# Optimization experiments

Hardware: AMD Instinct MI355X
Metric: run time of the kernel (lower is better)

## Reference

```python
import jax, jax.numpy as jnp
import numpy as np

B, D, H = 32768, 512, 512


def setup_inputs() -> dict:
    key = jax.random.key(0)
    ks = jax.random.split(key, 20)
    stdv = 1.0 / np.sqrt(H)

    def u(k, shape):
        return jax.random.uniform(k, shape, jnp.float32, -stdv, stdv)

    inp = {
        "input": jax.random.normal(ks[0], (B, D), jnp.float32),
        "h": jax.random.normal(ks[1], (B, H), jnp.float32),
        "c": jax.random.normal(ks[2], (B, H), jnp.float32),
    }
    names = ["w_ii", "w_hi", "b_ii", "b_hi", "w_if", "w_hf", "b_if", "b_hf",
             "w_ig", "w_hg", "b_ig", "b_hg", "w_io", "w_ho", "b_io", "b_ho"]
    shapes = {"w_i": (D, H), "w_h": (H, H), "b_": (H,)}
    for i, n in enumerate(names):
        shp = (D, H) if n.startswith("w_i") else ((H, H) if n.startswith("w_h") else (H,))
        inp[n] = u(ks[3 + i], shp)
    return inp


def lstm_cell(input, h, c,
              w_ii, w_hi, b_ii, b_hi, w_if, w_hf, b_if, b_hf,
              w_ig, w_hg, b_ig, b_hg, w_io, w_ho, b_io, b_ho):
    # Fuse the 8 small GEMMs into 2 concatenated GEMMs: [B,D]@[D,4H], [B,H]@[H,4H].
    w_x = jnp.concatenate([w_ii, w_if, w_ig, w_io], axis=1)   # [D, 4H]
    w_h = jnp.concatenate([w_hi, w_hf, w_hg, w_ho], axis=1)   # [H, 4H]
    b = jnp.concatenate([b_ii + b_hi, b_if + b_hf, b_ig + b_hg, b_io + b_ho])  # [4H]
    pre = input @ w_x + h @ w_h + b                            # [B, 4H]
    i, f, g, o = jnp.split(pre, 4, axis=1)
    i = jax.nn.sigmoid(i)
    f = jax.nn.sigmoid(f)
    g = jax.nn.sigmoid(g)  # NOTE: source code uses sigmoid here (docstring says tanh)
    o = jax.nn.sigmoid(o)
    c_prime = f * c + i * g
    h_prime = o * jnp.tanh(c_prime)
    return h_prime, c_prime


def reference(input, h, c,
              w_ii, w_hi, b_ii, b_hi, w_if, w_hf, b_if, b_hf,
              w_ig, w_hg, b_ig, b_hg, w_io, w_ho, b_io, b_ho):
    return lstm_cell(input, h, c,
                     w_ii, w_hi, b_ii, b_hi, w_if, w_hf, b_if, b_hf,
                     w_ig, w_hg, b_ig, b_hg, w_io, w_ho, b_io, b_ho)
```

## Files before the change

kernel.cpp:

```cpp
#include <hip/hip_runtime.h>
#include <hip/hip_bf16.h>

typedef __attribute__((ext_vector_type(8))) __bf16 bf16x8;
typedef __attribute__((ext_vector_type(4))) float f32x4;

#define NB 32768
#define HDIM 512
#define KDIM 1024

struct WPtrs { const float* wi[4]; const float* wh[4]; };
struct BPtrs { const float* bi[4]; const float* bh[4]; };

__device__ __forceinline__ float fsigmoid(float x) {
  return 1.0f / (1.0f + __expf(-x));
}
__device__ __forceinline__ float ftanh(float x) {
  return 2.0f / (1.0f + __expf(-2.0f * x)) - 1.0f;
}
__device__ __forceinline__ bf16x8 pack8(float4 a, float4 b) {
  bf16x8 r;
  r[0] = (__bf16)a.x; r[1] = (__bf16)a.y; r[2] = (__bf16)a.z; r[3] = (__bf16)a.w;
  r[4] = (__bf16)b.x; r[5] = (__bf16)b.y; r[6] = (__bf16)b.z; r[7] = (__bf16)b.w;
  return r;
}
__device__ __forceinline__ void gll16(const void* g, void* l) {
  __builtin_amdgcn_global_load_lds(
      (const __attribute__((address_space(1))) void*)g,
      (__attribute__((address_space(3))) void*)l, 16, 0, 0);
}
#define MFMA16(A, B, C) \
  C = __builtin_amdgcn_mfma_f32_16x16x32_bf16(A, B, C, 0, 0, 0)
#define SBAR() __builtin_amdgcn_s_barrier()
#define SCHED0() __builtin_amdgcn_sched_barrier(0)

__global__ void pack_bias_kernel(BPtrs p, float* __restrict__ bias) {
  int idx = blockIdx.x * 256 + threadIdx.x;
  int g = idx >> 9, np = idx & 511;
  bias[idx] = p.bi[g][np] + p.bh[g][np];
}

__global__ void conv_a_kernel(const float* __restrict__ x,
                              const float* __restrict__ h,
                              __bf16* __restrict__ Abf) {
  const size_t N8 = (size_t)NB * KDIM / 8;
  for (size_t i = (size_t)blockIdx.x * blockDim.x + threadIdx.x; i < N8;
       i += (size_t)gridDim.x * blockDim.x) {
    size_t e = i * 8;
    int k = (int)(e & (KDIM - 1));
    size_t r = e >> 10;
    const float* s = (k < 512) ? (x + r * 512 + k) : (h + r * 512 + (k - 512));
    float4 v0 = *(const float4*)s;
    float4 v1 = *(const float4*)(s + 4);
    *(bf16x8*)(Abf + e) = pack8(v0, v1);
  }
}

__global__ void pack_w2_kernel(WPtrs p, __bf16* __restrict__ Wt) {
  __shared__ float tile[64][65];
  const int kt = blockIdx.x;
  const int nt = blockIdx.y;
  const int g = blockIdx.z;
  const int k0 = kt * 64, n0 = nt * 64;
  const float* src = (k0 < 512) ? p.wi[g] : p.wh[g];
  const int k0l = (k0 < 512) ? k0 : (k0 - 512);
  const int rr = threadIdx.x >> 6;
  const int cc = threadIdx.x & 63;
#pragma unroll
  for (int pp = 0; pp < 16; ++pp) {
    int kk = pp * 4 + rr;
    tile[kk][cc] = src[(size_t)(k0l + kk) * 512 + (n0 + cc)];
  }
  __syncthreads();
#pragma unroll
  for (int pp = 0; pp < 16; ++pp) {
    int nn = pp * 4 + rr;
    int np = n0 + nn;
    int prow = (np >> 6) * 256 + ((g >> 1) << 7) + (((np >> 4) & 3) << 5) +
               ((g & 1) << 4) + (np & 15);
    Wt[(size_t)prow * KDIM + (k0 + cc)] = (__bf16)tile[cc][nn];
  }
}

__global__ __launch_bounds__(512, 1) void lstm_gemm6(
    const __bf16* __restrict__ Abf, const __bf16* __restrict__ Wt,
    const float* __restrict__ cin, const float* __restrict__ bias,
    float* __restrict__ out) {
  __shared__ alignas(16) char lds[131072];
  const int tid = threadIdx.x;
  const int wid = tid >> 6;
  const int wm = wid >> 2, wn = wid & 3;
  const int lane = tid & 63;
  const int fc = lane & 15, fg = lane >> 4;

  const int bn = blockIdx.x & 7;
  const int bmg = blockIdx.x >> 3;

  const __bf16* Bsrc = Wt + (size_t)(bn * 256) * KDIM;

  const int srow = (wid << 4) + (lane >> 2);
  const int skoff = (lane & 3) * 8;

  f32x4 acc[8][4];
#pragma unroll
  for (int m = 0; m < 8; ++m)
#pragma unroll
    for (int n = 0; n < 4; ++n) acc[m][n] = (f32x4){0.f, 0.f, 0.f, 0.f};

  bf16x8 a[2], b[4];

  auto stA = [&](int t) {
    if (t < 128) {
      const __bf16* s = Abf +
                        ((size_t)((bmg << 2) + (t >> 5)) * 256 + srow) * KDIM +
                        (t & 31) * 32 + skoff;
      uint32_t lb = (uint32_t)(t & 3) * 32768 + (uint32_t)wid * 1024;
      gll16(s, (void*)&lds[lb]);
      gll16(s + (size_t)128 * KDIM, (void*)&lds[lb + 8192]);
    }
  };
  auto stB = [&](int t) {
    if (t < 128) {
      const __bf16* s = Bsrc + (size_t)srow * KDIM + (t & 31) * 32 + skoff;
      uint32_t lb = (uint32_t)(t & 3) * 32768 + 16384 + (uint32_t)wid * 1024;
      gll16(s, (void*)&lds[lb]);
      gll16(s + (size_t)128 * KDIM, (void*)&lds[lb + 8192]);
    }
  };
  auto ldA = [&](uint32_t t3, int mq) -> bf16x8 {
    return *(const bf16x8*)&lds[t3 +
                                (uint32_t)(wm * 128 + mq * 16 + fc) * 64 +
                                (uint32_t)fg * 16];
  };
  auto ldB = [&](uint32_t t3, int nq) -> bf16x8 {
    return *(const bf16x8*)&lds[t3 + 16384 +
                                (uint32_t)((nq >> 1) * 128 + wn * 32 +
                                           (nq & 1) * 16 + fc) * 64 +
                                (uint32_t)fg * 16];
  };

  const int np = bn * 64 + wn * 16 + fc;
  const float bi = bias[np];
  const float bf_ = bias[512 + np];
  const float bg = bias[1024 + np];
  const float bo = bias[1536 + np];
  const size_t couts = (size_t)NB * HDIM;

  stA(0); stB(0); stA(1); stB(1);
  asm volatile("s_waitcnt vmcnt(4)" ::: "memory");
  SBAR();

#pragma unroll 4
  for (int t = 0; t < 128; ++t) {
    const uint32_t t3 = (uint32_t)(t & 3) * 32768;
    a[0] = ldA(t3, 0);
    b[0] = ldB(t3, 0);
    b[1] = ldB(t3, 1);
    b[2] = ldB(t3, 2);
    b[3] = ldB(t3, 3);
    a[1] = ldA(t3, 1);
#pragma unroll
    for (int mq = 0; mq < 8; ++mq) {
      if (mq < 7) {
        asm volatile("s_waitcnt lgkmcnt(1)" ::: "memory");
      } else {
        asm volatile("s_waitcnt lgkmcnt(0)" ::: "memory");
      }
      SCHED0();
      __builtin_amdgcn_s_setprio(1);
      MFMA16(a[mq & 1], b[0], acc[mq][0]);
      MFMA16(a[mq & 1], b[1], acc[mq][1]);
      MFMA16(a[mq & 1], b[2], acc[mq][2]);
      MFMA16(a[mq & 1], b[3], acc[mq][3]);
      __builtin_amdgcn_s_setprio(0);
      if (mq < 6) a[mq & 1] = ldA(t3, mq + 2);
      if (mq == 2) stA(t + 2);
      if (mq == 4) stB(t + 2);
    }
    if (t < 126) {
      asm volatile("s_waitcnt vmcnt(4)" ::: "memory");
    } else if (t == 126) {
      asm volatile("s_waitcnt vmcnt(0)" ::: "memory");
    }
    SBAR();

    if ((t & 31) == 31) {
      const int grp = t >> 5;
#pragma unroll
      for (int mf = 0; mf < 8; ++mf) {
        const int grow0 = ((bmg << 2) + grp) * 256 + wm * 128 + mf * 16 + fg * 4;
#pragma unroll
        for (int j = 0; j < 4; ++j) {
          const size_t off = (size_t)(grow0 + j) * HDIM + np;
          float i_ = fsigmoid(acc[mf][0][j] + bi);
          float f_ = fsigmoid(acc[mf][1][j] + bf_);
          float g_ = fsigmoid(acc[mf][2][j] + bg);
          float o_ = fsigmoid(acc[mf][3][j] + bo);
          float cp = f_ * cin[off] + i_ * g_;
          out[off] = o_ * ftanh(cp);
          out[couts + off] = cp;
        }
#pragma unroll
        for (int n = 0; n < 4; ++n) acc[mf][n] = (f32x4){0.f, 0.f, 0.f, 0.f};
      }
    }
  }
}

extern "C" void kernel_launch(void* const* d_in, const int* in_sizes, int n_in,
                              void* d_out, int out_size, void* d_ws,
                              size_t ws_size, hipStream_t stream) {
  const float* xin = (const float*)d_in[0];
  const float* hin = (const float*)d_in[1];
  const float* cin = (const float*)d_in[2];
  WPtrs wp;
  wp.wi[0] = (const float*)d_in[3];
  wp.wi[1] = (const float*)d_in[7];
  wp.wi[2] = (const float*)d_in[11];
  wp.wi[3] = (const float*)d_in[15];
  wp.wh[0] = (const float*)d_in[4];
  wp.wh[1] = (const float*)d_in[8];
  wp.wh[2] = (const float*)d_in[12];
  wp.wh[3] = (const float*)d_in[16];
  BPtrs bp;
  bp.bi[0] = (const float*)d_in[5];
  bp.bi[1] = (const float*)d_in[9];
  bp.bi[2] = (const float*)d_in[13];
  bp.bi[3] = (const float*)d_in[17];
  bp.bh[0] = (const float*)d_in[6];
  bp.bh[1] = (const float*)d_in[10];
  bp.bh[2] = (const float*)d_in[14];
  bp.bh[3] = (const float*)d_in[18];

  const size_t needA = (size_t)NB * KDIM * 2;
  const size_t needW = (size_t)2048 * KDIM * 2;

  __bf16* Abf = (__bf16*)d_ws;
  __bf16* Wt = (__bf16*)((char*)d_ws + needA);
  float* bias = (float*)((char*)d_ws + needA + needW);

  conv_a_kernel<<<2048, 256, 0, stream>>>(xin, hin, Abf);
  pack_w2_kernel<<<dim3(16, 8, 4), 256, 0, stream>>>(wp, Wt);
  pack_bias_kernel<<<8, 256, 0, stream>>>(bp, bias);
  lstm_gemm6<<<256, 512, 0, stream>>>(Abf, Wt, cin, bias, (float*)d_out);
}
```

Baseline: 213.8 us.

## Retile LSTM GEMM to 128x128 blocks with swizzled LDS and two blocks per CU

Measured after the change: 232.7 us. 1.09x slower.

```diff
diff --git a/kernel.cpp b/kernel.cpp
--- a/kernel.cpp
+++ b/kernel.cpp
@@ -32,6 +32,7 @@
   C = __builtin_amdgcn_mfma_f32_16x16x32_bf16(A, B, C, 0, 0, 0)
 #define SBAR() __builtin_amdgcn_s_barrier()
 #define SCHED0() __builtin_amdgcn_sched_barrier(0)
+#define LGKM(n) asm volatile("s_waitcnt lgkmcnt(" #n ")" ::: "memory")
 
 __global__ void pack_bias_kernel(BPtrs p, float* __restrict__ bias) {
   int idx = blockIdx.x * 256 + threadIdx.x;
@@ -55,7 +56,7 @@
   }
 }
 
-__global__ void pack_w2_kernel(WPtrs p, __bf16* __restrict__ Wt) {
+__global__ void pack_w3_kernel(WPtrs p, __bf16* __restrict__ Wt) {
   __shared__ float tile[64][65];
   const int kt = blockIdx.x;
   const int nt = blockIdx.y;
@@ -75,119 +76,147 @@
   for (int pp = 0; pp < 16; ++pp) {
     int nn = pp * 4 + rr;
     int np = n0 + nn;
-    int prow = (np >> 6) * 256 + ((g >> 1) << 7) + (((np >> 4) & 3) << 5) +
-               ((g & 1) << 4) + (np & 15);
+    int prow = ((np >> 4) << 6) + (g << 4) + (np & 15);
     Wt[(size_t)prow * KDIM + (k0 + cc)] = (__bf16)tile[cc][nn];
   }
 }
 
-__global__ __launch_bounds__(512, 1) void lstm_gemm6(
+__global__ __launch_bounds__(256, 2) void lstm_gemm7(
     const __bf16* __restrict__ Abf, const __bf16* __restrict__ Wt,
     const float* __restrict__ cin, const float* __restrict__ bias,
     float* __restrict__ out) {
-  __shared__ alignas(16) char lds[131072];
+  __shared__ alignas(16) char lds[65536];
   const int tid = threadIdx.x;
   const int wid = tid >> 6;
-  const int wm = wid >> 2, wn = wid & 3;
+  const int wm = wid >> 1, wn = wid & 1;
   const int lane = tid & 63;
   const int fc = lane & 15, fg = lane >> 4;
 
-  const int bn = blockIdx.x & 7;
-  const int bmg = blockIdx.x >> 3;
-
-  const __bf16* Bsrc = Wt + (size_t)(bn * 256) * KDIM;
-
-  const int srow = (wid << 4) + (lane >> 2);
-  const int skoff = (lane & 3) * 8;
-
-  f32x4 acc[8][4];
-#pragma unroll
-  for (int m = 0; m < 8; ++m)
+  const int bn = blockIdx.x & 15;
+  const int bmg = blockIdx.x >> 4;
+
+  const __bf16* Bsrc = Wt + (size_t)(bn * 128) * KDIM;
+
+  const int r0 = tid >> 3;
+  const int ssl = ((tid & 7) ^ (r0 & 7)) * 8;
+  const uint32_t ldst0 = (uint32_t)wid * 1024;
+
+  f32x4 acc[4][4];
+#pragma unroll
+  for (int m = 0; m < 4; ++m)
 #pragma unroll
     for (int n = 0; n < 4; ++n) acc[m][n] = (f32x4){0.f, 0.f, 0.f, 0.f};
 
-  bf16x8 a[2], b[4];
+  bf16x8 a0[4], b0[4], a1[4], b1[4];
 
   auto stA = [&](int t) {
     if (t < 128) {
-      const __bf16* s = Abf +
-                        ((size_t)((bmg << 2) + (t >> 5)) * 256 + srow) * KDIM +
-                        (t & 31) * 32 + skoff;
-      uint32_t lb = (uint32_t)(t & 3) * 32768 + (uint32_t)wid * 1024;
+      const int rt = (bmg << 3) + (t >> 4);
+      const __bf16* s =
+          Abf + (size_t)(rt * 128 + r0) * KDIM + (t & 15) * 64 + ssl;
+      uint32_t lb = (uint32_t)(t & 1) * 32768 + ldst0;
       gll16(s, (void*)&lds[lb]);
-      gll16(s + (size_t)128 * KDIM, (void*)&lds[lb + 8192]);
+      gll16(s + (size_t)32 * KDIM, (void*)&lds[lb + 4096]);
+      gll16(s + (size_t)64 * KDIM, (void*)&lds[lb + 8192]);
+      gll16(s + (size_t)96 * KDIM, (void*)&lds[lb + 12288]);
     }
   };
   auto stB = [&](int t) {
     if (t < 128) {
-      const __bf16* s = Bsrc + (size_t)srow * KDIM + (t & 31) * 32 + skoff;
-      uint32_t lb = (uint32_t)(t & 3) * 32768 + 16384 + (uint32_t)wid * 1024;
+      const __bf16* s = Bsrc + (size_t)r0 * KDIM + (t & 15) * 64 + ssl;
+      uint32_t lb = (uint32_t)(t & 1) * 32768 + 16384 + ldst0;
       gll16(s, (void*)&lds[lb]);
-      gll16(s + (size_t)128 * KDIM, (void*)&lds[lb + 8192]);
+      gll16(s + (size_t)32 * KDIM, (void*)&lds[lb + 4096]);
+      gll16(s + (size_t)64 * KDIM, (void*)&lds[lb + 8192]);
+      gll16(s + (size_t)96 * KDIM, (void*)&lds[lb + 12288]);
     }
   };
-  auto ldA = [&](uint32_t t3, int mq) -> bf16x8 {
-    return *(const bf16x8*)&lds[t3 +
-                                (uint32_t)(wm * 128 + mq * 16 + fc) * 64 +
-                                (uint32_t)fg * 16];
-  };
-  auto ldB = [&](uint32_t t3, int nq) -> bf16x8 {
-    return *(const bf16x8*)&lds[t3 + 16384 +
-                                (uint32_t)((nq >> 1) * 128 + wn * 32 +
-                                           (nq & 1) * 16 + fc) * 64 +
-                                (uint32_t)fg * 16];
-  };
-
-  const int np = bn * 64 + wn * 16 + fc;
+  auto ldA = [&](int cb, int mq, int ks) -> bf16x8 {
+    int row = wm * 64 + mq * 16 + fc;
+    uint32_t off = (uint32_t)cb * 32768 + (uint32_t)row * 128 +
+                   (uint32_t)(((ks * 4 + fg) ^ (row & 7)) << 4);
+    return *(const bf16x8*)&lds[off];
+  };
+  auto ldB = [&](int cb, int nq, int ks) -> bf16x8 {
+    int row = wn * 64 + nq * 16 + fc;
+    uint32_t off = (uint32_t)cb * 32768 + 16384 + (uint32_t)row * 128 +
+                   (uint32_t)(((ks * 4 + fg) ^ (row & 7)) << 4);
+    return *(const bf16x8*)&lds[off];
+  };
+
+  const int np = bn * 32 + wn * 16 + fc;
   const float bi = bias[np];
   const float bf_ = bias[512 + np];
   const float bg = bias[1024 + np];
   const float bo = bias[1536 + np];
   const size_t couts = (size_t)NB * HDIM;
 
-  stA(0); stB(0); stA(1); stB(1);
-  asm volatile("s_waitcnt vmcnt(4)" ::: "memory");
+  stA(0);
+  stB(0);
+  asm volatile("s_waitcnt vmcnt(0)" ::: "memory");
   SBAR();
 
-#pragma unroll 4
+#pragma unroll 2
   for (int t = 0; t < 128; ++t) {
-    const uint32_t t3 = (uint32_t)(t & 3) * 32768;
-    a[0] = ldA(t3, 0);
-    b[0] = ldB(t3, 0);
-    b[1] = ldB(t3, 1);
-    b[2] = ldB(t3, 2);
-    b[3] = ldB(t3, 3);
-    a[1] = ldA(t3, 1);
-#pragma unroll
-    for (int mq = 0; mq < 8; ++mq) {
-      if (mq < 7) {
-        asm volatile("s_waitcnt lgkmcnt(1)" ::: "memory");
-      } else {
-        asm volatile("s_waitcnt lgkmcnt(0)" ::: "memory");
-      }
-      SCHED0();
-      __builtin_amdgcn_s_setprio(1);
-      MFMA16(a[mq & 1], b[0], acc[mq][0]);
-      MFMA16(a[mq & 1], b[1], acc[mq][1]);
-      MFMA16(a[mq & 1], b[2], acc[mq][2]);
-      MFMA16(a[mq & 1], b[3], acc[mq][3]);
-      __builtin_amdgcn_s_setprio(0);
-      if (mq < 6) a[mq & 1] = ldA(t3, mq + 2);
-      if (mq == 2) stA(t + 2);
-      if (mq == 4) stB(t + 2);
-    }
-    if (t < 126) {
-      asm volatile("s_waitcnt vmcnt(4)" ::: "memory");
-    } else if (t == 126) {
-      asm volatile("s_waitcnt vmcnt(0)" ::: "memory");
-    }
+    const int cb = t & 1;
+    b0[0] = ldB(cb, 0, 0); b0[1] = ldB(cb, 1, 0);
+    b0[2] = ldB(cb, 2, 0); b0[3] = ldB(cb, 3, 0);
+    a0[0] = ldA(cb, 0, 0); a0[1] = ldA(cb, 1, 0);
+    a0[2] = ldA(cb, 2, 0); a0[3] = ldA(cb, 3, 0);
+    b1[0] = ldB(cb, 0, 1); b1[1] = ldB(cb, 1, 1);
+    b1[2] = ldB(cb, 2, 1); b1[3] = ldB(cb, 3, 1);
+    a1[0] = ldA(cb, 0, 1); a1[1] = ldA(cb, 1, 1);
+    a1[2] = ldA(cb, 2, 1); a1[3] = ldA(cb, 3, 1);
+    LGKM(11); SCHED0();
+    __builtin_amdgcn_s_setprio(1);
+    MFMA16(a0[0], b0[0], acc[0][0]); MFMA16(a0[0], b0[1], acc[0][1]);
+    MFMA16(a0[0], b0[2], acc[0][2]); MFMA16(a0[0], b0[3], acc[0][3]);
+    __builtin_amdgcn_s_setprio(0);
+    LGKM(10); SCHED0();
+    __builtin_amdgcn_s_setprio(1);
+    MFMA16(a0[1], b0[0], acc[1][0]); MFMA16(a0[1], b0[1], acc[1][1]);
+    MFMA16(a0[1], b0[2], acc[1][2]); MFMA16(a0[1], b0[3], acc[1][3]);
+    __builtin_amdgcn_s_setprio(0);
+    stA(t + 1);
+    LGKM(9); SCHED0();
+    __builtin_amdgcn_s_setprio(1);
+    MFMA16(a0[2], b0[0], acc[2][0]); MFMA16(a0[2], b0[1], acc[2][1]);
+    MFMA16(a0[2], b0[2], acc[2][2]); MFMA16(a0[2], b0[3], acc[2][3]);
+    __builtin_amdgcn_s_setprio(0);
+    LGKM(8); SCHED0();
+    __builtin_amdgcn_s_setprio(1);
+    MFMA16(a0[3], b0[0], acc[3][0]); MFMA16(a0[3], b0[1], acc[3][1]);
+    MFMA16(a0[3], b0[2], acc[3][2]); MFMA16(a0[3], b0[3], acc[3][3]);
+    __builtin_amdgcn_s_setprio(0);
+    stB(t + 1);
+    LGKM(3); SCHED0();
+    __builtin_amdgcn_s_setprio(1);
+    MFMA16(a1[0], b1[0], acc[0][0]); MFMA16(a1[0], b1[1], acc[0][1]);
+    MFMA16(a1[0], b1[2], acc[0][2]); MFMA16(a1[0], b1[3], acc[0][3]);
+    __builtin_amdgcn_s_setprio(0);
+    LGKM(2); SCHED0();
+    __builtin_amdgcn_s_setprio(1);
+    MFMA16(a1[1], b1[0], acc[1][0]); MFMA16(a1[1], b1[1], acc[1][1]);
+    MFMA16(a1[1], b1[2], acc[1][2]); MFMA16(a1[1], b1[3], acc[1][3]);
+    __builtin_amdgcn_s_setprio(0);
+    LGKM(1); SCHED0();
+    __builtin_amdgcn_s_setprio(1);
+    MFMA16(a1[2], b1[0], acc[2][0]); MFMA16(a1[2], b1[1], acc[2][1]);
+    MFMA16(a1[2], b1[2], acc[2][2]); MFMA16(a1[2], b1[3], acc[2][3]);
+    __builtin_amdgcn_s_setprio(0);
+    LGKM(0); SCHED0();
+    __builtin_amdgcn_s_setprio(1);
+    MFMA16(a1[3], b1[0], acc[3][0]); MFMA16(a1[3], b1[1], acc[3][1]);
+    MFMA16(a1[3], b1[2], acc[3][2]); MFMA16(a1[3], b1[3], acc[3][3]);
+    __builtin_amdgcn_s_setprio(0);
+    asm volatile("s_waitcnt vmcnt(0)" ::: "memory");
     SBAR();
 
-    if ((t & 31) == 31) {
-      const int grp = t >> 5;
-#pragma unroll
-      for (int mf = 0; mf < 8; ++mf) {
-        const int grow0 = ((bmg << 2) + grp) * 256 + wm * 128 + mf * 16 + fg * 4;
+    if ((t & 15) == 15) {
+      const int rt = (bmg << 3) + (t >> 4);
+#pragma unroll
+      for (int mf = 0; mf < 4; ++mf) {
+        const int grow0 = rt * 128 + wm * 64 + mf * 16 + fg * 4;
 #pragma unroll
         for (int j = 0; j < 4; ++j) {
           const size_t off = (size_t)(grow0 + j) * HDIM + np;
@@ -239,7 +268,7 @@
   float* bias = (float*)((char*)d_ws + needA + needW);
 
   conv_a_kernel<<<2048, 256, 0, stream>>>(xin, hin, Abf);
-  pack_w2_kernel<<<dim3(16, 8, 4), 256, 0, stream>>>(wp, Wt);
+  pack_w3_kernel<<<dim3(16, 8, 4), 256, 0, stream>>>(wp, Wt);
   pack_bias_kernel<<<8, 256, 0, stream>>>(bp, bias);
-  lstm_gemm6<<<256, 512, 0, stream>>>(Abf, Wt, cin, bias, (float*)d_out);
-}
+  lstm_gemm7<<<512, 256, 0, stream>>>(Abf, Wt, cin, bias, (float*)d_out);
+}
```
